# Performance work log

Measured on AMD Instinct MI355X. Metric: run time of the kernel, lower is better.

The kernel has to match this reference:

```python
import jax, jax.numpy as jnp
import numpy as np

N, E, F_IN, H, C, G = 50000, 800000, 128, 4, 32, 512
HC = H * C  # 128
EPS = 1e-5


def seg_mean(x, seg, num):
    s = jax.ops.segment_sum(x, seg, num_segments=num)
    cnt = jax.ops.segment_sum(jnp.ones((x.shape[0],), x.dtype), seg, num_segments=num)
    return s / jnp.maximum(cnt, 1.0)[:, None]


def graph_norm(x, batch, w, b, ms, num):
    # PyG GraphNorm: out = w * (x - mean_scale*mean_g) / sqrt(var_g + eps) + b
    mean = seg_mean(x, batch, num)
    out = x - mean[batch] * ms
    var = seg_mean(out * out, batch, num)
    std = jnp.sqrt(var + EPS)
    return w * out / std[batch] + b


def gatv2(x, Wl, bl, Wr, br, att, bias, src, dst, heads, ch, concat, n):
    xl = (x @ Wl + bl).reshape(n, heads, ch)
    xr = (x @ Wr + br).reshape(n, heads, ch)
    e = jax.nn.leaky_relu(xl[src] + xr[dst], 0.2)          # [E, H, C]
    logit = jnp.einsum('ehc,hc->eh', e, att)               # [E, H]
    m = jax.ops.segment_max(logit, dst, num_segments=n)
    ex = jnp.exp(logit - m[dst])
    den = jax.ops.segment_sum(ex, dst, num_segments=n)
    alpha = ex / den[dst]                                  # segment softmax over dst
    out = jax.ops.segment_sum(xl[src] * alpha[:, :, None], dst, num_segments=n)
    out = out.reshape(n, heads * ch) if concat else out.mean(axis=1)
    return out + bias


def setup_inputs() -> dict:
    key = jax.random.key(0)
    ks = jax.random.split(key, 32)
    def w(k, shape, fan_in):
        return jax.random.normal(k, shape, dtype=jnp.float32) / np.sqrt(fan_in)
    inp = {}
    inp['x'] = jax.random.normal(ks[0], (N, F_IN), dtype=jnp.float32)
    inp['edge_index'] = jax.random.randint(ks[1], (2, E), 0, N)
    inp['batch'] = jnp.sort(jax.random.randint(ks[2], (N,), 0, G))
    # conv1: GATv2Conv(F_IN -> C, heads=H, concat)
    inp['Wl1'] = w(ks[3], (F_IN, HC), F_IN); inp['bl1'] = jnp.zeros((HC,), jnp.float32)
    inp['Wr1'] = w(ks[4], (F_IN, HC), F_IN); inp['br1'] = jnp.zeros((HC,), jnp.float32)
    inp['att1'] = w(ks[5], (H, C), C); inp['bias1'] = jnp.zeros((HC,), jnp.float32)
    inp['gn1_w'] = jnp.ones((HC,), jnp.float32); inp['gn1_b'] = jnp.zeros((HC,), jnp.float32)
    inp['gn1_ms'] = jnp.ones((HC,), jnp.float32)
    # conv2: GATv2Conv(HC -> C, heads=1, concat=False)
    inp['Wl2'] = w(ks[6], (HC, C), HC); inp['bl2'] = jnp.zeros((C,), jnp.float32)
    inp['Wr2'] = w(ks[7], (HC, C), HC); inp['br2'] = jnp.zeros((C,), jnp.float32)
    inp['att2'] = w(ks[8], (1, C), C); inp['bias2'] = jnp.zeros((C,), jnp.float32)
    inp['gn2_w'] = jnp.ones((C,), jnp.float32); inp['gn2_b'] = jnp.zeros((C,), jnp.float32)
    inp['gn2_ms'] = jnp.ones((C,), jnp.float32)
    # residual projections
    inp['Wp1'] = w(ks[9], (F_IN, HC), F_IN); inp['bp1'] = jnp.zeros((HC,), jnp.float32)
    inp['Wp2'] = w(ks[10], (HC, C), HC); inp['bp2'] = jnp.zeros((C,), jnp.float32)
    # ego gate and heads
    inp['Weg'] = w(ks[11], (C, 2 * C), C); inp['beg'] = jnp.zeros((2 * C,), jnp.float32)
    inp['Wf1'] = w(ks[12], (3 * C, C), 3 * C); inp['bf1'] = jnp.zeros((C,), jnp.float32)
    inp['Wf2'] = w(ks[13], (C, 1), C); inp['bf2'] = jnp.zeros((1,), jnp.float32)
    return inp


def reference(x, edge_index, batch, Wl1, bl1, Wr1, br1, att1, bias1, gn1_w, gn1_b, gn1_ms,
              Wl2, bl2, Wr2, br2, att2, bias2, gn2_w, gn2_b, gn2_ms,
              Wp1, bp1, Wp2, bp2, Weg, beg, Wf1, bf1, Wf2, bf2):
    n = x.shape[0]
    loop = jnp.arange(n)
    src = jnp.concatenate([edge_index[0], loop])  # add_self_loops=True (PyG default)
    dst = jnp.concatenate([edge_index[1], loop])
    res1 = x @ Wp1 + bp1
    x1 = gatv2(x, Wl1, bl1, Wr1, br1, att1, bias1, src, dst, H, C, True, n)
    x1 = graph_norm(x1, batch, gn1_w, gn1_b, gn1_ms, G)
    h = jax.nn.gelu(x1 + res1, approximate=False)
    res2 = h @ Wp2 + bp2
    x2 = gatv2(h, Wl2, bl2, Wr2, br2, att2, bias2, src, dst, 1, C, False, n)
    x2 = graph_norm(x2, batch, gn2_w, gn2_b, gn2_ms, G)
    h = jax.nn.gelu(x2 + res2, approximate=False)
    x_mean = seg_mean(h, batch, G)
    cnt = jax.ops.segment_sum(jnp.ones((n,), h.dtype), batch, num_segments=G)
    x_max = jax.ops.segment_max(h, batch, num_segments=G)
    x_max = jnp.where(cnt[:, None] > 0, x_max, 0.0)
    x_root = x_mean  # no root_node attribute -> global_mean_pool
    gate = jax.nn.sigmoid(x_root @ Weg + beg)
    x_neigh = gate * jnp.concatenate([x_mean, x_max], axis=1)
    x_final = jnp.concatenate([x_root, x_neigh], axis=1)  # [G, 3C]
    emb = jax.nn.gelu(x_final @ Wf1 + bf1, approximate=False)
    return emb @ Wf2 + bf2
```

## Files before the change

kernel.cpp:

```cpp
#include <hip/hip_runtime.h>
#include <math.h>

#define EPS 1e-5f

__device__ __forceinline__ float gelu_exact(float v) {
    return 0.5f * v * (1.0f + erff(v * 0.70710678118654752f));
}

__global__ void seg_bounds_k(const int* __restrict__ batch, int N, int G, int* __restrict__ seg) {
    int i = blockIdx.x * blockDim.x + threadIdx.x;
    if (i >= N) return;
    int b = batch[i];
    if (i == 0) {
        for (int g = 0; g <= b; ++g) seg[g] = 0;
    } else {
        int pb = batch[i - 1];
        for (int g = pb + 1; g <= b; ++g) seg[g] = i;
    }
    if (i == N - 1) {
        for (int g = b + 1; g <= G; ++g) seg[g] = N;
    }
}

__global__ void hist_k(const int* __restrict__ ei, int E, int Etot, int* __restrict__ cnt) {
    int e = blockIdx.x * blockDim.x + threadIdx.x;
    if (e >= Etot) return;
    int dst = (e < E) ? ei[E + e] : (e - E);
    atomicAdd(&cnt[dst], 1);
}

__global__ void scan_k(const int* __restrict__ cnt, int N, int* __restrict__ rowptr) {
    __shared__ int ts[1024];
    int t = threadIdx.x;
    int chunk = (N + 1023) / 1024;
    int s0 = t * chunk;
    int e0 = min(s0 + chunk, N);
    int sum = 0;
    for (int i = s0; i < e0; ++i) sum += cnt[i];
    ts[t] = sum;
    __syncthreads();
    for (int off = 1; off < 1024; off <<= 1) {
        int v = (t >= off) ? ts[t - off] : 0;
        __syncthreads();
        ts[t] += v;
        __syncthreads();
    }
    int run = (t > 0) ? ts[t - 1] : 0;
    for (int i = s0; i < e0; ++i) {
        rowptr[i] = run;
        run += cnt[i];
    }
    if (t == 1023) rowptr[N] = ts[1023];
}

__global__ void scatter_k(const int* __restrict__ ei, int E, int Etot,
                          const int* __restrict__ rowptr, int* __restrict__ cur,
                          int* __restrict__ esrc) {
    int e = blockIdx.x * blockDim.x + threadIdx.x;
    if (e >= Etot) return;
    int src, dst;
    if (e < E) { src = ei[e]; dst = ei[E + e]; }
    else       { src = e - E; dst = src; }
    int pos = rowptr[dst] + atomicAdd(&cur[dst], 1);
    esrc[pos] = src;
}

template <int K, int M>
__global__ void linear3_k(const float* __restrict__ A,
                          const float* __restrict__ W0, const float* __restrict__ b0,
                          const float* __restrict__ W1, const float* __restrict__ b1,
                          const float* __restrict__ W2, const float* __restrict__ b2,
                          float* __restrict__ o0, float* __restrict__ o1,
                          float* __restrict__ o2, int nrows) {
    constexpr int ROWS = 32;
    constexpr int NG = 256 / M;
    constexpr int RPT = ROWS / NG;
    __shared__ float lds[ROWS * K];
    int row0 = blockIdx.x * ROWS;
    int t = threadIdx.x;
    for (int idx = t; idx < ROWS * K / 4; idx += 256) {
        int r = idx / (K / 4), c4 = idx % (K / 4);
        int row = row0 + r;
        float4 v = make_float4(0.f, 0.f, 0.f, 0.f);
        if (row < nrows) v = *reinterpret_cast<const float4*>(&A[(long)row * K + c4 * 4]);
        *reinterpret_cast<float4*>(&lds[r * K + c4 * 4]) = v;
    }
    __syncthreads();
    int c = t % M, g = t / M;
    float a0[RPT], a1[RPT], a2[RPT];
    float bv0 = b0[c], bv1 = b1[c], bv2 = b2[c];
#pragma unroll
    for (int r = 0; r < RPT; ++r) { a0[r] = bv0; a1[r] = bv1; a2[r] = bv2; }
    for (int k = 0; k < K; ++k) {
        float w0 = W0[k * M + c], w1 = W1[k * M + c], w2 = W2[k * M + c];
#pragma unroll
        for (int r = 0; r < RPT; ++r) {
            float xv = lds[(g * RPT + r) * K + k];
            a0[r] += xv * w0; a1[r] += xv * w1; a2[r] += xv * w2;
        }
    }
#pragma unroll
    for (int r = 0; r < RPT; ++r) {
        int row = row0 + g * RPT + r;
        if (row < nrows) {
            o0[(long)row * M + c] = a0[r];
            o1[(long)row * M + c] = a1[r];
            o2[(long)row * M + c] = a2[r];
        }
    }
}

__global__ void __launch_bounds__(256) gat1_k(
        const float* __restrict__ xl, const float* __restrict__ xr,
        const float* __restrict__ att, const int* __restrict__ rowptr,
        const int* __restrict__ esrc, float* __restrict__ outp, int N) {
    int node = blockIdx.x * 2 + (threadIdx.x >> 7);
    if (node >= N) return;
    int f = threadIdx.x & 127;
    float xrf = xr[(long)node * 128 + f];
    float af = att[f];
    int s = rowptr[node], e = rowptr[node + 1];
    float m = -INFINITY, den = 0.f, acc = 0.f;
    int i = s;
    for (; i + 4 <= e; i += 4) {
        int s0 = esrc[i], s1 = esrc[i + 1], s2 = esrc[i + 2], s3 = esrc[i + 3];
        float x0 = xl[(long)s0 * 128 + f];
        float x1 = xl[(long)s1 * 128 + f];
        float x2 = xl[(long)s2 * 128 + f];
        float x3 = xl[(long)s3 * 128 + f];
        float v0 = x0 + xrf; v0 = ((v0 > 0.f) ? v0 : 0.2f * v0) * af;
        float v1 = x1 + xrf; v1 = ((v1 > 0.f) ? v1 : 0.2f * v1) * af;
        float v2 = x2 + xrf; v2 = ((v2 > 0.f) ? v2 : 0.2f * v2) * af;
        float v3 = x3 + xrf; v3 = ((v3 > 0.f) ? v3 : 0.2f * v3) * af;
#pragma unroll
        for (int off = 16; off > 0; off >>= 1) {
            v0 += __shfl_xor(v0, off, 32);
            v1 += __shfl_xor(v1, off, 32);
            v2 += __shfl_xor(v2, off, 32);
            v3 += __shfl_xor(v3, off, 32);
        }
        float vm = fmaxf(fmaxf(v0, v1), fmaxf(v2, v3));
        float nm = fmaxf(m, vm);
        float sc = __expf(m - nm);
        float p0 = __expf(v0 - nm), p1 = __expf(v1 - nm);
        float p2 = __expf(v2 - nm), p3 = __expf(v3 - nm);
        den = den * sc + ((p0 + p1) + (p2 + p3));
        acc = acc * sc + ((p0 * x0 + p1 * x1) + (p2 * x2 + p3 * x3));
        m = nm;
    }
    for (; i < e; ++i) {
        int srcn = esrc[i];
        float xlv = xl[(long)srcn * 128 + f];
        float v = xlv + xrf;
        v = ((v > 0.f) ? v : 0.2f * v) * af;
#pragma unroll
        for (int off = 16; off > 0; off >>= 1) v += __shfl_xor(v, off, 32);
        float nm = fmaxf(m, v);
        float sc = __expf(m - nm);
        float p  = __expf(v - nm);
        den = den * sc + p;
        acc = acc * sc + p * xlv;
        m = nm;
    }
    outp[(long)node * 128 + f] = acc / den;
}

__global__ void __launch_bounds__(256) gat2_k(
        const float* __restrict__ xl, const float* __restrict__ xr,
        const float* __restrict__ att, const int* __restrict__ rowptr,
        const int* __restrict__ esrc, float* __restrict__ outp, int N) {
    int node = blockIdx.x * 8 + (threadIdx.x >> 5);
    if (node >= N) return;
    int f = threadIdx.x & 31;
    float xrf = xr[(long)node * 32 + f];
    float af = att[f];
    int s = rowptr[node], e = rowptr[node + 1];
    float m = -INFINITY, den = 0.f, acc = 0.f;
    int i = s;
    for (; i + 4 <= e; i += 4) {
        int s0 = esrc[i], s1 = esrc[i + 1], s2 = esrc[i + 2], s3 = esrc[i + 3];
        float x0 = xl[(long)s0 * 32 + f];
        float x1 = xl[(long)s1 * 32 + f];
        float x2 = xl[(long)s2 * 32 + f];
        float x3 = xl[(long)s3 * 32 + f];
        float v0 = x0 + xrf; v0 = ((v0 > 0.f) ? v0 : 0.2f * v0) * af;
        float v1 = x1 + xrf; v1 = ((v1 > 0.f) ? v1 : 0.2f * v1) * af;
        float v2 = x2 + xrf; v2 = ((v2 > 0.f) ? v2 : 0.2f * v2) * af;
        float v3 = x3 + xrf; v3 = ((v3 > 0.f) ? v3 : 0.2f * v3) * af;
#pragma unroll
        for (int off = 16; off > 0; off >>= 1) {
            v0 += __shfl_xor(v0, off, 32);
            v1 += __shfl_xor(v1, off, 32);
            v2 += __shfl_xor(v2, off, 32);
            v3 += __shfl_xor(v3, off, 32);
        }
        float vm = fmaxf(fmaxf(v0, v1), fmaxf(v2, v3));
        float nm = fmaxf(m, vm);
        float sc = __expf(m - nm);
        float p0 = __expf(v0 - nm), p1 = __expf(v1 - nm);
        float p2 = __expf(v2 - nm), p3 = __expf(v3 - nm);
        den = den * sc + ((p0 + p1) + (p2 + p3));
        acc = acc * sc + ((p0 * x0 + p1 * x1) + (p2 * x2 + p3 * x3));
        m = nm;
    }
    for (; i < e; ++i) {
        int srcn = esrc[i];
        float xlv = xl[(long)srcn * 32 + f];
        float v = xlv + xrf;
        v = ((v > 0.f) ? v : 0.2f * v) * af;
#pragma unroll
        for (int off = 16; off > 0; off >>= 1) v += __shfl_xor(v, off, 32);
        float nm = fmaxf(m, v);
        float sc = __expf(m - nm);
        float p  = __expf(v - nm);
        den = den * sc + p;
        acc = acc * sc + p * xlv;
        m = nm;
    }
    outp[(long)node * 32 + f] = acc / den;
}

template <int F, int NW>
__global__ void gn_stats_k(const float* __restrict__ x, const float* __restrict__ bias,
                           const float* __restrict__ ms, const int* __restrict__ seg,
                           float* __restrict__ meanp, float* __restrict__ istdp) {
    __shared__ float s1s[NW][F];
    __shared__ float s2s[NW][F];
    int g = blockIdx.x;
    int f = threadIdx.x % F, j = threadIdx.x / F;
    int s = seg[g], e = seg[g + 1];
    int count = e - s;
    float bv = bias[f];
    float s1 = 0.f, s2 = 0.f;
    for (int n = s + j; n < e; n += NW) {
        float v = x[(long)n * F + f] + bv;
        s1 += v;
        s2 += v * v;
    }
    s1s[j][f] = s1;
    s2s[j][f] = s2;
    __syncthreads();
    if (j == 0) {
#pragma unroll
        for (int jj = 1; jj < NW; ++jj) { s1 += s1s[jj][f]; s2 += s2s[jj][f]; }
        float cnt = (float)max(count, 1);
        float mean = s1 / cnt;
        float mms = mean * ms[f];
        float var = s2 / cnt - 2.f * mms * mean + mms * mms;
        meanp[(long)g * F + f] = mean;
        istdp[(long)g * F + f] = 1.0f / sqrtf(var + EPS);
    }
}

template <int F>
__global__ void gn_apply_k(const float* __restrict__ x, const float* __restrict__ bias,
                           const int* __restrict__ batch, const float* __restrict__ meanp,
                           const float* __restrict__ istdp, const float* __restrict__ w,
                           const float* __restrict__ b, const float* __restrict__ ms,
                           const float* __restrict__ res, float* __restrict__ h, int N) {
    constexpr int F4 = F / 4;
    long i = (long)blockIdx.x * blockDim.x + threadIdx.x;
    if (i >= (long)N * F4) return;
    int n = (int)(i / F4), f4 = (int)(i % F4);
    int g = batch[n];
    long base = (long)n * F + f4 * 4;
    long gbase = (long)g * F + f4 * 4;
    float4 xv = *reinterpret_cast<const float4*>(&x[base]);
    float4 rv = *reinterpret_cast<const float4*>(&res[base]);
    float4 mv = *reinterpret_cast<const float4*>(&meanp[gbase]);
    float4 iv = *reinterpret_cast<const float4*>(&istdp[gbase]);
    float4 bv = *reinterpret_cast<const float4*>(&bias[f4 * 4]);
    float4 wv = *reinterpret_cast<const float4*>(&w[f4 * 4]);
    float4 bb = *reinterpret_cast<const float4*>(&b[f4 * 4]);
    float4 mw = *reinterpret_cast<const float4*>(&ms[f4 * 4]);
    float4 o;
    o.x = gelu_exact(wv.x * ((xv.x + bv.x) - mv.x * mw.x) * iv.x + bb.x + rv.x);
    o.y = gelu_exact(wv.y * ((xv.y + bv.y) - mv.y * mw.y) * iv.y + bb.y + rv.y);
    o.z = gelu_exact(wv.z * ((xv.z + bv.z) - mv.z * mw.z) * iv.z + bb.z + rv.z);
    o.w = gelu_exact(wv.w * ((xv.w + bv.w) - mv.w * mw.w) * iv.w + bb.w + rv.w);
    *reinterpret_cast<float4*>(&h[base]) = o;
}

__global__ void pool_head_k(const float* __restrict__ h2, const int* __restrict__ seg,
                            const float* __restrict__ Weg, const float* __restrict__ beg,
                            const float* __restrict__ Wf1, const float* __restrict__ bf1,
                            const float* __restrict__ Wf2, const float* __restrict__ bf2,
                            float* __restrict__ outp) {
    int g = blockIdx.x, t = threadIdx.x;
    int s = seg[g], epos = seg[g + 1];
    int count = epos - s;
    __shared__ float ssum[8][32];
    __shared__ float smax[8][32];
    __shared__ float xfinal[96];
    __shared__ float emb[32];
    int f = t % 32, j = t / 32;
    float sum = 0.f, mx = -INFINITY;
    for (int n = s + j; n < epos; n += 8) {
        float v = h2[(long)n * 32 + f];
        sum += v;
        mx = fmaxf(mx, v);
    }
    ssum[j][f] = sum;
    smax[j][f] = mx;
    __syncthreads();
    if (t < 32) {
        float acs = 0.f, acm = -INFINITY;
        for (int jj = 0; jj < 8; ++jj) { acs += ssum[jj][t]; acm = fmaxf(acm, smax[jj][t]); }
        float mean = acs / (float)max(count, 1);
        float mxv = (count > 0) ? acm : 0.0f;
        xfinal[t] = mean;
        smax[0][t] = mxv;
    }
    __syncthreads();
    if (t < 64) {
        float acc = beg[t];
        for (int k = 0; k < 32; ++k) acc += xfinal[k] * Weg[k * 64 + t];
        float gate = 1.0f / (1.0f + expf(-acc));
        float val = (t < 32) ? xfinal[t] : smax[0][t - 32];
        xfinal[32 + t] = gate * val;
    }
    __syncthreads();
    if (t < 32) {
        float acc = bf1[t];
        for (int k = 0; k < 96; ++k) acc += xfinal[k] * Wf1[k * 32 + t];
        emb[t] = gelu_exact(acc);
    }
    __syncthreads();
    if (t < 32) {
        float v = emb[t] * Wf2[t];
#pragma unroll
        for (int off = 16; off > 0; off >>= 1) v += __shfl_xor(v, off, 32);
        if (t == 0) outp[g] = v + bf2[0];
    }
}

extern "C" void kernel_launch(void* const* d_in, const int* in_sizes, int n_in, void* d_out,
                              int out_size, void* d_ws, size_t ws_size, hipStream_t stream) {
    const float* x      = (const float*)d_in[0];
    const int*   ei     = (const int*)d_in[1];
    const int*   batch  = (const int*)d_in[2];
    const float* Wl1    = (const float*)d_in[3];
    const float* bl1    = (const float*)d_in[4];
    const float* Wr1    = (const float*)d_in[5];
    const float* br1    = (const float*)d_in[6];
    const float* att1   = (const float*)d_in[7];
    const float* bias1  = (const float*)d_in[8];
    const float* gn1_w  = (const float*)d_in[9];
    const float* gn1_b  = (const float*)d_in[10];
    const float* gn1_ms = (const float*)d_in[11];
    const float* Wl2    = (const float*)d_in[12];
    const float* bl2    = (const float*)d_in[13];
    const float* Wr2    = (const float*)d_in[14];
    const float* br2    = (const float*)d_in[15];
    const float* att2   = (const float*)d_in[16];
    const float* bias2  = (const float*)d_in[17];
    const float* gn2_w  = (const float*)d_in[18];
    const float* gn2_b  = (const float*)d_in[19];
    const float* gn2_ms = (const float*)d_in[20];
    const float* Wp1    = (const float*)d_in[21];
    const float* bp1    = (const float*)d_in[22];
    const float* Wp2    = (const float*)d_in[23];
    const float* bp2    = (const float*)d_in[24];
    const float* Weg    = (const float*)d_in[25];
    const float* beg    = (const float*)d_in[26];
    const float* Wf1    = (const float*)d_in[27];
    const float* bf1    = (const float*)d_in[28];
    const float* Wf2    = (const float*)d_in[29];
    const float* bf2    = (const float*)d_in[30];
    float* outp = (float*)d_out;

    const int N = in_sizes[2];
    const int E = in_sizes[1] / 2;
    const int Etot = E + N;
    const int G = out_size;
    constexpr int HC = 128, C = 32;

    char* ws = (char*)d_ws;
    size_t off = 0;
    auto alloc = [&](size_t bytes) -> void* {
        void* p = ws + off;
        off += (bytes + 255) & ~(size_t)255;
        return p;
    };
    int*   seg    = (int*)alloc((size_t)(G + 1) * 4);
    int*   cnt    = (int*)alloc((size_t)N * 4);
    int*   cur    = (int*)alloc((size_t)N * 4);
    int*   rowptr = (int*)alloc((size_t)(N + 1) * 4);
    int*   esrc   = (int*)alloc((size_t)Etot * 4);
    float* xl1    = (float*)alloc((size_t)N * HC * 4);
    float* xr1    = (float*)alloc((size_t)N * HC * 4);
    float* res1   = (float*)alloc((size_t)N * HC * 4);
    float* out1   = (float*)alloc((size_t)N * HC * 4);
    float* mean1  = (float*)alloc((size_t)G * HC * 4);
    float* istd1  = (float*)alloc((size_t)G * HC * 4);
    float* xl2    = (float*)alloc((size_t)N * C * 4);
    float* xr2    = (float*)alloc((size_t)N * C * 4);
    float* res2   = (float*)alloc((size_t)N * C * 4);
    float* out2   = (float*)alloc((size_t)N * C * 4);
    float* h2     = (float*)alloc((size_t)N * C * 4);
    float* mean2  = (float*)alloc((size_t)G * C * 4);
    float* istd2  = (float*)alloc((size_t)G * C * 4);
    float* h1     = xl1;
    (void)ws_size; (void)n_in;

    seg_bounds_k<<<(N + 255) / 256, 256, 0, stream>>>(batch, N, G, seg);
    hipMemsetAsync(cnt, 0, (size_t)N * 4, stream);
    hipMemsetAsync(cur, 0, (size_t)N * 4, stream);
    hist_k<<<(Etot + 255) / 256, 256, 0, stream>>>(ei, E, Etot, cnt);
    scan_k<<<1, 1024, 0, stream>>>(cnt, N, rowptr);
    scatter_k<<<(Etot + 255) / 256, 256, 0, stream>>>(ei, E, Etot, rowptr, cur, esrc);

    int gblk = (N + 31) / 32;
    linear3_k<128, 128><<<gblk, 256, 0, stream>>>(x, Wl1, bl1, Wr1, br1, Wp1, bp1,
                                                  xl1, xr1, res1, N);
    gat1_k<<<(N + 1) / 2, 256, 0, stream>>>(xl1, xr1, att1, rowptr, esrc, out1, N);
    gn_stats_k<128, 4><<<G, 512, 0, stream>>>(out1, bias1, gn1_ms, seg, mean1, istd1);
    gn_apply_k<128><<<(int)(((long)N * 32 + 255) / 256), 256, 0, stream>>>(
        out1, bias1, batch, mean1, istd1, gn1_w, gn1_b, gn1_ms, res1, h1, N);

    linear3_k<128, 32><<<gblk, 256, 0, stream>>>(h1, Wl2, bl2, Wr2, br2, Wp2, bp2,
                                                 xl2, xr2, res2, N);
    gat2_k<<<(N + 7) / 8, 256, 0, stream>>>(xl2, xr2, att2, rowptr, esrc, out2, N);
    gn_stats_k<32, 16><<<G, 512, 0, stream>>>(out2, bias2, gn2_ms, seg, mean2, istd2);
    gn_apply_k<32><<<(int)(((long)N * 8 + 255) / 256), 256, 0, stream>>>(
        out2, bias2, batch, mean2, istd2, gn2_w, gn2_b, gn2_ms, res2, h2, N);

    pool_head_k<<<G, 256, 0, stream>>>(h2, seg, Weg, beg, Wf1, bf1, Wf2, bf2, outp);
}
```

Baseline: 621.5 us.

## Register-tile the fused triple linear with K-blocked shared-memory weights

Replaces the triple-output linear kernel with a register-blocked version. Each thread now computes a TM x 4 tile for all three weight matrices, and both the input rows and the weights are staged through shared memory in K chunks of 32. An XOR swizzle on the input tile avoids LDS bank conflicts. The goal is fewer redundant global weight loads and more FMAs per LDS read, at the cost of about 144 accumulator registers per thread, which may limit occupancy.

```diff
diff --git a/kernel.cpp b/kernel.cpp
--- a/kernel.cpp
+++ b/kernel.cpp
@@ -65,47 +65,103 @@
     esrc[pos] = src;
 }
 
-template <int K, int M>
-__global__ void linear3_k(const float* __restrict__ A,
-                          const float* __restrict__ W0, const float* __restrict__ b0,
-                          const float* __restrict__ W1, const float* __restrict__ b1,
-                          const float* __restrict__ W2, const float* __restrict__ b2,
-                          float* __restrict__ o0, float* __restrict__ o1,
-                          float* __restrict__ o2, int nrows) {
-    constexpr int ROWS = 32;
-    constexpr int NG = 256 / M;
-    constexpr int RPT = ROWS / NG;
-    __shared__ float lds[ROWS * K];
-    int row0 = blockIdx.x * ROWS;
+template <int M, int CGN, int RGN, int TM>
+__global__ void __launch_bounds__(CGN * RGN) linear3v2_k(
+        const float* __restrict__ A,
+        const float* __restrict__ W0, const float* __restrict__ b0,
+        const float* __restrict__ W1, const float* __restrict__ b1,
+        const float* __restrict__ W2, const float* __restrict__ b2,
+        float* __restrict__ o0, float* __restrict__ o1, float* __restrict__ o2,
+        int nrows) {
+    constexpr int K = 128;
+    constexpr int BK = 32;
+    constexpr int BM = RGN * TM;
+    constexpr int NT = CGN * RGN;
+    __shared__ float xs[BM * BK];
+    __shared__ float ws[3 * BK * M];
     int t = threadIdx.x;
-    for (int idx = t; idx < ROWS * K / 4; idx += 256) {
-        int r = idx / (K / 4), c4 = idx % (K / 4);
-        int row = row0 + r;
-        float4 v = make_float4(0.f, 0.f, 0.f, 0.f);
-        if (row < nrows) v = *reinterpret_cast<const float4*>(&A[(long)row * K + c4 * 4]);
-        *reinterpret_cast<float4*>(&lds[r * K + c4 * 4]) = v;
-    }
-    __syncthreads();
-    int c = t % M, g = t / M;
-    float a0[RPT], a1[RPT], a2[RPT];
-    float bv0 = b0[c], bv1 = b1[c], bv2 = b2[c];
-#pragma unroll
-    for (int r = 0; r < RPT; ++r) { a0[r] = bv0; a1[r] = bv1; a2[r] = bv2; }
-    for (int k = 0; k < K; ++k) {
-        float w0 = W0[k * M + c], w1 = W1[k * M + c], w2 = W2[k * M + c];
-#pragma unroll
-        for (int r = 0; r < RPT; ++r) {
-            float xv = lds[(g * RPT + r) * K + k];
-            a0[r] += xv * w0; a1[r] += xv * w1; a2[r] += xv * w2;
-        }
-    }
-#pragma unroll
-    for (int r = 0; r < RPT; ++r) {
-        int row = row0 + g * RPT + r;
-        if (row < nrows) {
-            o0[(long)row * M + c] = a0[r];
-            o1[(long)row * M + c] = a1[r];
-            o2[(long)row * M + c] = a2[r];
+    int row0 = blockIdx.x * BM;
+    int cg = t % CGN, rg = t / CGN;
+    int c0 = cg * 4;
+    int r0 = rg * TM;
+
+    float acc[3][TM][4];
+    {
+        float4 v0 = *reinterpret_cast<const float4*>(&b0[c0]);
+        float4 v1 = *reinterpret_cast<const float4*>(&b1[c0]);
+        float4 v2 = *reinterpret_cast<const float4*>(&b2[c0]);
+#pragma unroll
+        for (int r = 0; r < TM; ++r) {
+            acc[0][r][0] = v0.x; acc[0][r][1] = v0.y; acc[0][r][2] = v0.z; acc[0][r][3] = v0.w;
+            acc[1][r][0] = v1.x; acc[1][r][1] = v1.y; acc[1][r][2] = v1.z; acc[1][r][3] = v1.w;
+            acc[2][r][0] = v2.x; acc[2][r][1] = v2.y; acc[2][r][2] = v2.z; acc[2][r][3] = v2.w;
+        }
+    }
+
+    for (int k0 = 0; k0 < K; k0 += BK) {
+        if (k0) __syncthreads();
+        for (int idx = t; idx < BM * 8; idx += NT) {
+            int r = idx >> 3, j = idx & 7;
+            int grow = row0 + r;
+            float4 v = make_float4(0.f, 0.f, 0.f, 0.f);
+            if (grow < nrows) v = *reinterpret_cast<const float4*>(&A[(long)grow * K + k0 + j * 4]);
+            int swz = (r ^ (r >> 3)) & 7;
+            *reinterpret_cast<float4*>(&xs[r * BK + ((j ^ swz) << 2)]) = v;
+        }
+        for (int idx = t; idx < BK * (M / 4); idx += NT) {
+            int kk = idx / (M / 4), c4 = idx % (M / 4);
+            long goff = (long)(k0 + kk) * M + c4 * 4;
+            int loff = kk * M + c4 * 4;
+            *reinterpret_cast<float4*>(&ws[loff]) =
+                *reinterpret_cast<const float4*>(&W0[goff]);
+            *reinterpret_cast<float4*>(&ws[BK * M + loff]) =
+                *reinterpret_cast<const float4*>(&W1[goff]);
+            *reinterpret_cast<float4*>(&ws[2 * BK * M + loff]) =
+                *reinterpret_cast<const float4*>(&W2[goff]);
+        }
+        __syncthreads();
+
+#pragma unroll
+        for (int k4 = 0; k4 < BK; k4 += 4) {
+            float4 wv[3][4];
+#pragma unroll
+            for (int m = 0; m < 3; ++m)
+#pragma unroll
+                for (int kk = 0; kk < 4; ++kk)
+                    wv[m][kk] = *reinterpret_cast<const float4*>(
+                        &ws[m * BK * M + (k4 + kk) * M + c0]);
+#pragma unroll
+            for (int r = 0; r < TM; ++r) {
+                int rr = r0 + r;
+                int swz = (rr ^ (rr >> 3)) & 7;
+                float4 xv = *reinterpret_cast<const float4*>(
+                    &xs[rr * BK + (((k4 >> 2) ^ swz) << 2)]);
+#pragma unroll
+                for (int m = 0; m < 3; ++m) {
+                    acc[m][r][0] += xv.x * wv[m][0].x + xv.y * wv[m][1].x +
+                                    xv.z * wv[m][2].x + xv.w * wv[m][3].x;
+                    acc[m][r][1] += xv.x * wv[m][0].y + xv.y * wv[m][1].y +
+                                    xv.z * wv[m][2].y + xv.w * wv[m][3].y;
+                    acc[m][r][2] += xv.x * wv[m][0].z + xv.y * wv[m][1].z +
+                                    xv.z * wv[m][2].z + xv.w * wv[m][3].z;
+                    acc[m][r][3] += xv.x * wv[m][0].w + xv.y * wv[m][1].w +
+                                    xv.z * wv[m][2].w + xv.w * wv[m][3].w;
+                }
+            }
+        }
+    }
+
+#pragma unroll
+    for (int r = 0; r < TM; ++r) {
+        int grow = row0 + r0 + r;
+        if (grow < nrows) {
+            long o = (long)grow * M + c0;
+            *reinterpret_cast<float4*>(&o0[o]) =
+                make_float4(acc[0][r][0], acc[0][r][1], acc[0][r][2], acc[0][r][3]);
+            *reinterpret_cast<float4*>(&o1[o]) =
+                make_float4(acc[1][r][0], acc[1][r][1], acc[1][r][2], acc[1][r][3]);
+            *reinterpret_cast<float4*>(&o2[o]) =
+                make_float4(acc[2][r][0], acc[2][r][1], acc[2][r][2], acc[2][r][3]);
         }
     }
 }
@@ -410,16 +466,15 @@
     scan_k<<<1, 1024, 0, stream>>>(cnt, N, rowptr);
     scatter_k<<<(Etot + 255) / 256, 256, 0, stream>>>(ei, E, Etot, rowptr, cur, esrc);
 
-    int gblk = (N + 31) / 32;
-    linear3_k<128, 128><<<gblk, 256, 0, stream>>>(x, Wl1, bl1, Wr1, br1, Wp1, bp1,
-                                                  xl1, xr1, res1, N);
+    linear3v2_k<128, 32, 8, 8><<<(N + 63) / 64, 256, 0, stream>>>(
+        x, Wl1, bl1, Wr1, br1, Wp1, bp1, xl1, xr1, res1, N);
     gat1_k<<<(N + 1) / 2, 256, 0, stream>>>(xl1, xr1, att1, rowptr, esrc, out1, N);
     gn_stats_k<128, 4><<<G, 512, 0, stream>>>(out1, bias1, gn1_ms, seg, mean1, istd1);
     gn_apply_k<128><<<(int)(((long)N * 32 + 255) / 256), 256, 0, stream>>>(
         out1, bias1, batch, mean1, istd1, gn1_w, gn1_b, gn1_ms, res1, h1, N);
 
-    linear3_k<128, 32><<<gblk, 256, 0, stream>>>(h1, Wl2, bl2, Wr2, br2, Wp2, bp2,
-                                                 xl2, xr2, res2, N);
+    linear3v2_k<32, 8, 16, 8><<<(N + 127) / 128, 128, 0, stream>>>(
+        h1, Wl2, bl2, Wr2, br2, Wp2, bp2, xl2, xr2, res2, N);
     gat2_k<<<(N + 7) / 8, 256, 0, stream>>>(xl2, xr2, att2, rowptr, esrc, out2, N);
     gn_stats_k<32, 16><<<G, 512, 0, stream>>>(out2, bias2, gn2_ms, seg, mean2, istd2);
     gn_apply_k<32><<<(int)(((long)N * 8 + 255) / 256), 256, 0, stream>>>(
```

New measurement: 1.073 ms. +72.7%, slower.
